# Optimization experiments

Hardware: AMD Instinct MI355X
Metric: run time of the kernel (lower is better)

Reference implementation:

```python
import jax, jax.numpy as jnp
import numpy as np


def setup_inputs() -> dict:
    key = jax.random.key(0)
    k1, k2 = jax.random.split(key)
    n, h, L, d = 4, 16, 1024, 64
    max_positions = 512
    query = jax.random.normal(k1, (n, h, L, d), dtype=jnp.float32)
    rel_emb = jax.random.normal(k2, (h, d, 2 * max_positions + 1), dtype=jnp.float32)
    return {"query": query, "rel_emb": rel_emb, "length": L}


def reference(query, rel_emb, length):
    # logits: [n, h, i, 2*max_positions+1]
    logits = jnp.einsum('nhid,hdj->nhij', query, rel_emb)
    max_positions = (rel_emb.shape[-1] - 1) // 2
    idx = jnp.arange(length)
    # relative offsets grid [i, j] = j - i  (last=False path)
    grid = idx[None, :] - idx[:, None]
    # clamp to valid range and shift to table indices
    table_idx = jnp.clip(grid, 1 - max_positions, max_positions - 1) + max_positions
    n, h = logits.shape[0], logits.shape[1]
    gather_idx = jnp.broadcast_to(table_idx[None, None, :, :], (n, h, length, length))
    # out[n,h,i,j] = logits[n,h,i,table_idx[i,j]]
    out = jnp.take_along_axis(logits, gather_idx, axis=-1)
    return out
```

## Files before the change

### kernel.cpp

```cpp
#include <hip/hip_runtime.h>
#include <hip/hip_bf16.h>


#define NH 16
#define LQ 1024
#define DD 64
#define TT 1025
#define MAXP 512
#define RING 288
#define RSTRIDE 296

typedef float f32x4 __attribute__((ext_vector_type(4)));
typedef short s16x4 __attribute__((ext_vector_type(4)));
typedef short s16x8 __attribute__((ext_vector_type(8)));

__device__ __forceinline__ short f2bf(float f) {
    __hip_bfloat16 h = __float2bfloat16(f);
    return __builtin_bit_cast(short, h);
}
__device__ __forceinline__ float bf2f(unsigned short s) {
    return __builtin_bit_cast(float, ((unsigned)s) << 16);
}
__device__ __forceinline__ int mod288(int x) {
    return x >= 864 ? x - 864 : (x >= 576 ? x - 576 : (x >= 288 ? x - 288 : x));
}

template<int D>
__device__ __forceinline__ void write_row(const unsigned short* __restrict__ lrow,
                                          int i, int c, int l,
                                          float* __restrict__ orow) {
    const float p1 = bf2f(lrow[1]);
    const float p2 = bf2f(lrow[159]);
    const int j0 = c * 256 + 4 * l;
    const int t0 = j0 - i + MAXP;
    const int tA = t0 - D;
    int a = tA;     a = a < 0 ? 0 : (a > 1020 ? 1020 : a);
    int b = tA + 4; b = b < 0 ? 0 : (b > 1020 ? 1020 : b);
    const s16x4 A = *(const s16x4*)(lrow + mod288(a));
    const s16x4 B = *(const s16x4*)(lrow + mod288(b));
    f32x4 v;
    #pragma unroll
    for (int e = 0; e < 4; ++e) {
        const int t = t0 + e;
        const short in = (D + e < 4) ? A[D + e] : B[D + e - 4];
        v[e] = t < 1 ? p1 : (t > LQ - 1 ? p2 : bf2f((unsigned short)in));
    }
    __builtin_nontemporal_store(v, (f32x4*)(orow + j0));
}

__global__ __launch_bounds__(256, 4) void lpb_stream(const float* __restrict__ Q,
                                                     const float* __restrict__ R,
                                                     float* __restrict__ out) {
    __shared__ unsigned short lg[4][16][RSTRIDE];

    const int bidx = blockIdx.x;
    const int swz  = (bidx & 7) * 128 + (bidx >> 3);
    const int nh   = swz >> 4;
    const int rg   = swz & 15;
    const int h    = nh & (NH - 1);

    const int tid = threadIdx.x;
    const int w = tid >> 6, l = tid & 63;
    const int n = l & 15, g = l >> 4;
    const int base = rg * 64 + w * 16;
    unsigned short (*ring)[RSTRIDE] = lg[w];

    const float* qrow = Q + ((size_t)nh * LQ + (base + n)) * DD + 8 * g;
    s16x8 qf[2];
    #pragma unroll
    for (int kh = 0; kh < 2; ++kh) {
        f32x4 a = *(const f32x4*)(qrow + kh * 32);
        f32x4 b = *(const f32x4*)(qrow + kh * 32 + 4);
        #pragma unroll
        for (int r = 0; r < 4; ++r) { qf[kh][r] = f2bf(a[r]); qf[kh][4 + r] = f2bf(b[r]); }
    }

    const float* rbase = R + (size_t)(h * DD + 8 * g) * TT;
    float* obase = out + (size_t)nh * LQ * LQ;

    int computed = 0;
    int ringc = 0;

    #pragma unroll 1
    for (int c = 0; c < 4; ++c) {
        const int Thi = 256 * c + 767 - base;
        int need = (Thi + 16) >> 4;
        need = need < 1 ? 1 : (need > 64 ? 64 : need);

        #pragma unroll 1
        for (; computed < need; ++computed) {
            const int tb = computed << 4;
            const float* rc = rbase + tb + n;
            s16x8 rf0, rf1;
            #pragma unroll
            for (int r = 0; r < 8; ++r) {
                rf0[r] = f2bf(rc[(size_t)r * TT]);
                rf1[r] = f2bf(rc[(size_t)(32 + r) * TT]);
            }
            f32x4 acc = (f32x4){0.f, 0.f, 0.f, 0.f};
            acc = __builtin_amdgcn_mfma_f32_16x16x32_bf16(rf0, qf[0], acc, 0, 0, 0);
            acc = __builtin_amdgcn_mfma_f32_16x16x32_bf16(rf1, qf[1], acc, 0, 0, 0);
            s16x4 hv;
            #pragma unroll
            for (int s = 0; s < 4; ++s) hv[s] = f2bf(acc[s]);
            *(s16x4*)&ring[n][ringc + 4 * g] = hv;
            ringc += 16; if (ringc == RING) ringc = 0;
        }

        #pragma unroll 1
        for (int q = 0; q < 4; ++q) {
            { const int rr = ((2048 + MAXP - base - 0) & 3) + 4 * q; const int i = base + rr;
              write_row<0>(&ring[rr][0], i, c, l, obase + (size_t)i * LQ); }
            { const int rr = ((2048 + MAXP - base - 1) & 3) + 4 * q; const int i = base + rr;
              write_row<1>(&ring[rr][0], i, c, l, obase + (size_t)i * LQ); }
            { const int rr = ((2048 + MAXP - base - 2) & 3) + 4 * q; const int i = base + rr;
              write_row<2>(&ring[rr][0], i, c, l, obase + (size_t)i * LQ); }
            { const int rr = ((2048 + MAXP - base - 3) & 3) + 4 * q; const int i = base + rr;
              write_row<3>(&ring[rr][0], i, c, l, obase + (size_t)i * LQ); }
        }
    }
}

extern "C" void kernel_launch(void* const* d_in, const int* in_sizes, int n_in,
                              void* d_out, int out_size, void* d_ws, size_t ws_size,
                              hipStream_t stream) {
    const float* Q = (const float*)d_in[0];
    const float* R = (const float*)d_in[1];
    float* out = (float*)d_out;

    lpb_stream<<<dim3(1024), 256, 0, stream>>>(Q, R, out);
}
```

Baseline: 84.05 us.

## Share rel_emb fragments across batch dimension with two-slot LDS logits buffer

Each block now covers one head and 16 query rows for all 4 batch entries, so each loaded rel_emb fragment feeds four MFMA pairs instead of one. The per-wave 288-entry ring is replaced by a block-wide two-slot LDS buffer of 256-column chunks. Workgroup barriers separate compute from the output-streaming phase. In exchange it adds __syncthreads, doubles LDS use and register pressure (launch bounds drop to 2 blocks per SM), and computes only the needed chunk range per row block.

Measured after the change: 83.39 us. Within noise of the previous version (-0.8%).

```diff
diff --git a/kernel.cpp b/kernel.cpp
--- a/kernel.cpp
+++ b/kernel.cpp
@@ -7,8 +7,8 @@
 #define DD 64
 #define TT 1025
 #define MAXP 512
-#define RING 288
-#define RSTRIDE 296
+#define CST 264
+#define SSTR (64 * CST)
 
 typedef float f32x4 __attribute__((ext_vector_type(4)));
 typedef short s16x4 __attribute__((ext_vector_type(4)));
@@ -21,103 +21,108 @@
 __device__ __forceinline__ float bf2f(unsigned short s) {
     return __builtin_bit_cast(float, ((unsigned)s) << 16);
 }
-__device__ __forceinline__ int mod288(int x) {
-    return x >= 864 ? x - 864 : (x >= 576 ? x - 576 : (x >= 288 ? x - 288 : x));
-}
 
 template<int D>
-__device__ __forceinline__ void write_row(const unsigned short* __restrict__ lrow,
-                                          int i, int c, int l,
+__device__ __forceinline__ void write_row(const unsigned short* __restrict__ lgrow0,
+                                          int i, int OC, int l,
                                           float* __restrict__ orow) {
-    const float p1 = bf2f(lrow[1]);
-    const float p2 = bf2f(lrow[159]);
-    const int j0 = c * 256 + 4 * l;
+    const float p1 = bf2f(lgrow0[1]);
+    const float p2 = bf2f(lgrow0[SSTR + 255]);
+    const int j0 = OC * 256 + 4 * l;
     const int t0 = j0 - i + MAXP;
     const int tA = t0 - D;
-    int a = tA;     a = a < 0 ? 0 : (a > 1020 ? 1020 : a);
-    int b = tA + 4; b = b < 0 ? 0 : (b > 1020 ? 1020 : b);
-    const s16x4 A = *(const s16x4*)(lrow + mod288(a));
-    const s16x4 B = *(const s16x4*)(lrow + mod288(b));
+    int ta = tA     < 0 ? 0 : (tA     > 1020 ? 1020 : tA);
+    int tb = tA + 4 < 0 ? 0 : (tA + 4 > 1020 ? 1020 : tA + 4);
+    const s16x4 A = *(const s16x4*)(lgrow0 + ((ta >> 8) & 1) * SSTR + (ta & 255));
+    s16x4 Bv = A;
+    if (D) Bv = *(const s16x4*)(lgrow0 + ((tb >> 8) & 1) * SSTR + (tb & 255));
     f32x4 v;
     #pragma unroll
     for (int e = 0; e < 4; ++e) {
         const int t = t0 + e;
-        const short in = (D + e < 4) ? A[D + e] : B[D + e - 4];
-        v[e] = t < 1 ? p1 : (t > LQ - 1 ? p2 : bf2f((unsigned short)in));
+        const unsigned short in = (unsigned short)((D + e < 4) ? A[D + e] : Bv[D + e - 4]);
+        v[e] = t < 1 ? p1 : (t > LQ - 1 ? p2 : bf2f(in));
     }
     __builtin_nontemporal_store(v, (f32x4*)(orow + j0));
 }
 
-__global__ __launch_bounds__(256, 4) void lpb_stream(const float* __restrict__ Q,
+__global__ __launch_bounds__(256, 2) void lpb_nshare(const float* __restrict__ Q,
                                                      const float* __restrict__ R,
                                                      float* __restrict__ out) {
-    __shared__ unsigned short lg[4][16][RSTRIDE];
+    __shared__ unsigned short lg[2][64][CST];
 
     const int bidx = blockIdx.x;
     const int swz  = (bidx & 7) * 128 + (bidx >> 3);
-    const int nh   = swz >> 4;
-    const int rg   = swz & 15;
-    const int h    = nh & (NH - 1);
+    const int h    = swz >> 6;
+    const int ib   = swz & 63;
+    const int base = ib * 16;
 
     const int tid = threadIdx.x;
     const int w = tid >> 6, l = tid & 63;
     const int n = l & 15, g = l >> 4;
-    const int base = rg * 64 + w * 16;
-    unsigned short (*ring)[RSTRIDE] = lg[w];
 
-    const float* qrow = Q + ((size_t)nh * LQ + (base + n)) * DD + 8 * g;
-    s16x8 qf[2];
+    s16x8 qf[4][2];
     #pragma unroll
-    for (int kh = 0; kh < 2; ++kh) {
-        f32x4 a = *(const f32x4*)(qrow + kh * 32);
-        f32x4 b = *(const f32x4*)(qrow + kh * 32 + 4);
+    for (int nn = 0; nn < 4; ++nn) {
+        const float* qrow = Q + ((size_t)(nn * NH + h) * LQ + (base + n)) * DD + 8 * g;
         #pragma unroll
-        for (int r = 0; r < 4; ++r) { qf[kh][r] = f2bf(a[r]); qf[kh][4 + r] = f2bf(b[r]); }
+        for (int kh = 0; kh < 2; ++kh) {
+            f32x4 a = *(const f32x4*)(qrow + kh * 32);
+            f32x4 b = *(const f32x4*)(qrow + kh * 32 + 4);
+            #pragma unroll
+            for (int r = 0; r < 4; ++r) { qf[nn][kh][r] = f2bf(a[r]); qf[nn][kh][4 + r] = f2bf(b[r]); }
+        }
     }
 
-    const float* rbase = R + (size_t)(h * DD + 8 * g) * TT;
-    float* obase = out + (size_t)nh * LQ * LQ;
-
-    int computed = 0;
-    int ringc = 0;
+    const int klo   = (base <= 240) ? 1 : 0;
+    const int klast = min(3, (1535 - base) >> 8);
+    int ocn = 0;
 
     #pragma unroll 1
-    for (int c = 0; c < 4; ++c) {
-        const int Thi = 256 * c + 767 - base;
-        int need = (Thi + 16) >> 4;
-        need = need < 1 ? 1 : (need > 64 ? 64 : need);
-
-        #pragma unroll 1
-        for (; computed < need; ++computed) {
-            const int tb = computed << 4;
-            const float* rc = rbase + tb + n;
+    for (int k = klo; k <= klast; ++k) {
+        unsigned short (*slot)[CST] = lg[k & 1];
+        #pragma unroll
+        for (int mt = 0; mt < 4; ++mt) {
+            const int tb = (k << 8) + (w << 6) + (mt << 4);
+            const float* rc = R + (size_t)(h * DD + 8 * g) * TT + tb + n;
             s16x8 rf0, rf1;
             #pragma unroll
             for (int r = 0; r < 8; ++r) {
                 rf0[r] = f2bf(rc[(size_t)r * TT]);
                 rf1[r] = f2bf(rc[(size_t)(32 + r) * TT]);
             }
-            f32x4 acc = (f32x4){0.f, 0.f, 0.f, 0.f};
-            acc = __builtin_amdgcn_mfma_f32_16x16x32_bf16(rf0, qf[0], acc, 0, 0, 0);
-            acc = __builtin_amdgcn_mfma_f32_16x16x32_bf16(rf1, qf[1], acc, 0, 0, 0);
-            s16x4 hv;
+            const int col = (tb & 255) + 4 * g;
             #pragma unroll
-            for (int s = 0; s < 4; ++s) hv[s] = f2bf(acc[s]);
-            *(s16x4*)&ring[n][ringc + 4 * g] = hv;
-            ringc += 16; if (ringc == RING) ringc = 0;
+            for (int nn = 0; nn < 4; ++nn) {
+                f32x4 acc = (f32x4){0.f, 0.f, 0.f, 0.f};
+                acc = __builtin_amdgcn_mfma_f32_16x16x32_bf16(rf0, qf[nn][0], acc, 0, 0, 0);
+                acc = __builtin_amdgcn_mfma_f32_16x16x32_bf16(rf1, qf[nn][1], acc, 0, 0, 0);
+                s16x4 hv;
+                #pragma unroll
+                for (int s = 0; s < 4; ++s) hv[s] = f2bf(acc[s]);
+                *(s16x4*)&slot[nn * 16 + n][col] = hv;
+            }
         }
+        __syncthreads();
 
+        int ocmax = (k == klast) ? 3 : (((k << 8) + 255 - 767 + base) >> 8);
+        if (ocmax > 3) ocmax = 3;
         #pragma unroll 1
-        for (int q = 0; q < 4; ++q) {
-            { const int rr = ((2048 + MAXP - base - 0) & 3) + 4 * q; const int i = base + rr;
-              write_row<0>(&ring[rr][0], i, c, l, obase + (size_t)i * LQ); }
-            { const int rr = ((2048 + MAXP - base - 1) & 3) + 4 * q; const int i = base + rr;
-              write_row<1>(&ring[rr][0], i, c, l, obase + (size_t)i * LQ); }
-            { const int rr = ((2048 + MAXP - base - 2) & 3) + 4 * q; const int i = base + rr;
-              write_row<2>(&ring[rr][0], i, c, l, obase + (size_t)i * LQ); }
-            { const int rr = ((2048 + MAXP - base - 3) & 3) + 4 * q; const int i = base + rr;
-              write_row<3>(&ring[rr][0], i, c, l, obase + (size_t)i * LQ); }
+        for (; ocn <= ocmax; ++ocn) {
+            float* obase = out + (size_t)(w * NH + h) * LQ * LQ;
+            #pragma unroll 1
+            for (int q = 0; q < 4; ++q) {
+                { const int rl = ((2048 + MAXP - base - 0) & 3) + 4 * q; const int i = base + rl;
+                  write_row<0>(&lg[0][w * 16 + rl][0], i, ocn, l, obase + (size_t)i * LQ); }
+                { const int rl = ((2048 + MAXP - base - 1) & 3) + 4 * q; const int i = base + rl;
+                  write_row<1>(&lg[0][w * 16 + rl][0], i, ocn, l, obase + (size_t)i * LQ); }
+                { const int rl = ((2048 + MAXP - base - 2) & 3) + 4 * q; const int i = base + rl;
+                  write_row<2>(&lg[0][w * 16 + rl][0], i, ocn, l, obase + (size_t)i * LQ); }
+                { const int rl = ((2048 + MAXP - base - 3) & 3) + 4 * q; const int i = base + rl;
+                  write_row<3>(&lg[0][w * 16 + rl][0], i, ocn, l, obase + (size_t)i * LQ); }
+            }
         }
+        __syncthreads();
     }
 }
 
@@ -128,5 +133,5 @@
     const float* R = (const float*)d_in[1];
     float* out = (float*)d_out;
 
-    lpb_stream<<<dim3(1024), 256, 0, stream>>>(Q, R, out);
+    lpb_nshare<<<dim3(1024), 256, 0, stream>>>(Q, R, out);
 }
```
